# Optimization experiments

Measured on AMD Instinct MI355X. Metric: run time of the kernel, lower is better.

## Reference

```python
import jax, jax.numpy as jnp
from jax import lax
import numpy as np

T, B, IN, H = 512, 256, 128, 512
TAU_MIN, TAU_MAX, DT = 0.2, 2.0, 0.1


def setup_inputs() -> dict:
    key = jax.random.key(0)
    ks = jax.random.split(key, 7)
    s_zh = 1.0 / np.sqrt(IN + H)  # torch Linear default init scale (fan_in)
    s_h = 1.0 / np.sqrt(H)
    return {
        "x_seq": jax.random.normal(ks[0], (T, B, IN), dtype=jnp.float32),
        "Wc": jax.random.uniform(ks[1], (IN + H, H), jnp.float32, -s_zh, s_zh),
        "bc": jax.random.uniform(ks[2], (H,), jnp.float32, -s_zh, s_zh),
        "Wt": jax.random.uniform(ks[3], (IN + H, H), jnp.float32, -s_zh, s_zh),
        "bt": jax.random.uniform(ks[4], (H,), jnp.float32, -s_zh, s_zh),
        "Wo": jax.random.uniform(ks[5], (H, 1), jnp.float32, -s_h, s_h),
        "bo": jax.random.uniform(ks[6], (1,), jnp.float32, -s_h, s_h),
    }


def reference(x_seq, Wc, bc, Wt, bt, Wo, bo):
    # Liquid time-constant RNN: sequential scan over T timesteps.
    def step(h, x_t):
        z = jnp.concatenate([x_t, h], axis=-1)           # [B, IN+H]
        candidate = jnp.tanh(z @ Wc + bc)                # [B, H]
        tau = TAU_MIN + jax.nn.sigmoid(z @ Wt + bt) * (TAU_MAX - TAU_MIN)
        h_next = h + DT * (-h + candidate) / tau         # ODE Euler update
        y_t = h_next @ Wo + bo                           # [B, 1]
        return h_next, (y_t, tau)

    h0 = jnp.zeros((x_seq.shape[1], Wc.shape[1]), dtype=x_seq.dtype)
    _, (y_seq, tau_seq) = lax.scan(step, h0, x_seq)
    return y_seq, tau_seq
```

## Files before the change

### kernel.cpp

```cpp
#include <hip/hip_runtime.h>
#include <stdint.h>

#define T_STEPS 512
#define BATCH   256
#define INP     128
#define HID     512
#define BGN     16
#define CGN     8
#define RB      16
#define CB      64
#define ZP      648

typedef float f32x4 __attribute__((ext_vector_type(4)));
typedef short s16x8 __attribute__((ext_vector_type(8)));
typedef unsigned short u16;
typedef unsigned int   u32;
typedef unsigned long long u64;

__device__ __forceinline__ u32 f2bf(float f) {
  union { float f; u32 u; } v; v.f = f;
  return (v.u + 0x7fffu + ((v.u >> 16) & 1u)) >> 16;
}

__device__ __forceinline__ float bf2f(u16 b) {
  union { u32 u; float f; } v; v.u = ((u32)b) << 16;
  return v.f;
}


__global__ __launch_bounds__(256, 1)
void liquid_persistent(const float* __restrict__ x_seq,
                       const float* __restrict__ Wc, const float* __restrict__ bc,
                       const float* __restrict__ Wt, const float* __restrict__ bt,
                       const float* __restrict__ Wo, const float* __restrict__ bo,
                       float* __restrict__ y_out, float* __restrict__ tau_out,
                       u16* __restrict__ hb)
{
  const int tid  = threadIdx.x;
  const int l    = tid & 63;
  const int w    = tid >> 6;
  const int quad = l >> 4;
  const int ln   = l & 15;
  const int bg   = blockIdx.x & (BGN - 1);
  const int cg   = blockIdx.x >> 4;
  const int R0   = bg * RB;
  const int C0   = cg * CB;
  const int cn   = C0 + w * 16 + ln;

  __shared__ u16 zS[RB][ZP];
  __shared__ float ypS[4];

  s16x8 wfC[20], wfT[20];
#pragma unroll
  for (int kt = 0; kt < 20; ++kt) {
#pragma unroll
    for (int j = 0; j < 8; ++j) {
      int k = kt * 32 + quad * 8 + j;
      wfC[kt][j] = (short)f2bf(Wc[k * HID + cn]);
      wfT[kt][j] = (short)f2bf(Wt[k * HID + cn]);
    }
  }

  const float bcv = bc[cn], btv = bt[cn];
  const float bov = bo[0];
  float hm[4] = {0.f, 0.f, 0.f, 0.f};

  const int xrow = tid >> 4;
  const int xseg = tid & 15;

  const int yrow = 2 * cg + (w >> 1);
  const int yc0  = (w & 1) * 256 + l * 4;
  const float4 wo4 = *(const float4*)&Wo[yc0];

  int ii[7];
#pragma unroll
  for (int jx = 0; jx < 7; ++jx) ii[jx] = jx + (jx >= cg ? 1 : 0);

  const size_t rowq = HID / 4;
  u64* hbase = (u64*)(void*)hb;
  const size_t myrow = (size_t)(R0 + xrow) * rowq;

  {
    const float* xp = x_seq + ((size_t)0 * BATCH + R0 + xrow) * INP + xseg * 8;
    float4 a = *(const float4*)xp;
    float4 b = *(const float4*)(xp + 4);
    u64 w0 = (u64)f2bf(a.x) | ((u64)f2bf(a.y) << 16) |
             ((u64)f2bf(a.z) << 32) | ((u64)f2bf(a.w) << 48);
    u64 w1 = (u64)f2bf(b.x) | ((u64)f2bf(b.y) << 16) |
             ((u64)f2bf(b.z) << 32) | ((u64)f2bf(b.w) << 48);
    *(u64*)&zS[xrow][xseg * 8]     = w0;
    *(u64*)&zS[xrow][xseg * 8 + 4] = w1;
  }
  __syncthreads();

  for (int t = 0; t <= T_STEPS; ++t) {
    const u64* rbase = hbase + (size_t)(t & 3) * BATCH * rowq + myrow + xseg;

    u64 tmp[7];
    if (t > 0) {
#pragma unroll
      for (int jx = 0; jx < 7; ++jx)
        tmp[jx] = __hip_atomic_load(rbase + ii[jx] * 16, __ATOMIC_RELAXED,
                                    __HIP_MEMORY_SCOPE_AGENT);
    }

    f32x4 aC0 = {0.f,0.f,0.f,0.f}, aC1 = {0.f,0.f,0.f,0.f};
    f32x4 aT0 = {0.f,0.f,0.f,0.f}, aT1 = {0.f,0.f,0.f,0.f};
    const u16* zb = &zS[ln][quad * 8];
    if (t < T_STEPS) {
      s16x8 a0 = *(const s16x8*)(zb);
      s16x8 a1 = *(const s16x8*)(zb + 32);
      s16x8 a2 = *(const s16x8*)(zb + 64);
      s16x8 a3 = *(const s16x8*)(zb + 96);
      aC0 = __builtin_amdgcn_mfma_f32_16x16x32_bf16(a0, wfC[0], aC0, 0,0,0);
      aT0 = __builtin_amdgcn_mfma_f32_16x16x32_bf16(a0, wfT[0], aT0, 0,0,0);
      aC1 = __builtin_amdgcn_mfma_f32_16x16x32_bf16(a1, wfC[1], aC1, 0,0,0);
      aT1 = __builtin_amdgcn_mfma_f32_16x16x32_bf16(a1, wfT[1], aT1, 0,0,0);
      aC0 = __builtin_amdgcn_mfma_f32_16x16x32_bf16(a2, wfC[2], aC0, 0,0,0);
      aT0 = __builtin_amdgcn_mfma_f32_16x16x32_bf16(a2, wfT[2], aT0, 0,0,0);
      aC1 = __builtin_amdgcn_mfma_f32_16x16x32_bf16(a3, wfC[3], aC1, 0,0,0);
      aT1 = __builtin_amdgcn_mfma_f32_16x16x32_bf16(a3, wfT[3], aT1, 0,0,0);
    }

    u64 hv[7];
    if (t == 0) {
#pragma unroll
      for (int jx = 0; jx < 7; ++jx) hv[jx] = 0;
    } else {
      bool need[7];
      int pending = 0;
#pragma unroll
      for (int jx = 0; jx < 7; ++jx) {
        u64 v = tmp[jx];
        bool ok = ((u32)v != 0xFFFFFFFFu) && ((u32)(v >> 32) != 0xFFFFFFFFu);
        hv[jx] = v;
        need[jx] = !ok;
        pending += ok ? 0 : 1;
      }
      while (pending) {
#pragma unroll
        for (int jx = 0; jx < 7; ++jx)
          if (need[jx])
            tmp[jx] = __hip_atomic_load(rbase + ii[jx] * 16, __ATOMIC_RELAXED,
                                        __HIP_MEMORY_SCOPE_AGENT);
#pragma unroll
        for (int jx = 0; jx < 7; ++jx)
          if (need[jx]) {
            u64 v = tmp[jx];
            if (((u32)v != 0xFFFFFFFFu) && ((u32)(v >> 32) != 0xFFFFFFFFu)) {
              hv[jx] = v;
              need[jx] = false;
              --pending;
            }
          }
      }
    }

    if (t < T_STEPS) {
      u64* pp = hbase + (size_t)((t + 2) & 3) * BATCH * rowq + myrow
              + (C0 / 4 + xseg);
      __hip_atomic_store(pp, ~0ull, __ATOMIC_RELAXED, __HIP_MEMORY_SCOPE_AGENT);
    }

    float4 xr0, xr1;
    if (t < T_STEPS) {
      const int tn = (t + 1 < T_STEPS) ? t + 1 : t;
      const float* xp = x_seq + ((size_t)tn * BATCH + R0 + xrow) * INP + xseg * 8;
      xr0 = *(const float4*)xp;
      xr1 = *(const float4*)(xp + 4);
    }

#pragma unroll
    for (int jx = 0; jx < 7; ++jx)
      *(u64*)&zS[xrow][INP + (ii[jx] * 16 + xseg) * 4] = hv[jx];
#pragma unroll
    for (int r = 0; r < 4; ++r)
      zS[quad * 4 + r][INP + cn] = (u16)f2bf(hm[r]);

    __syncthreads();

    float tauv[4];
    if (t < T_STEPS) {
#pragma unroll
      for (int kt = 4; kt < 20; kt += 2) {
        s16x8 a0 = *(const s16x8*)(zb + kt * 32);
        s16x8 a1 = *(const s16x8*)(zb + kt * 32 + 32);
        aC0 = __builtin_amdgcn_mfma_f32_16x16x32_bf16(a0, wfC[kt],   aC0, 0,0,0);
        aT0 = __builtin_amdgcn_mfma_f32_16x16x32_bf16(a0, wfT[kt],   aT0, 0,0,0);
        aC1 = __builtin_amdgcn_mfma_f32_16x16x32_bf16(a1, wfC[kt+1], aC1, 0,0,0);
        aT1 = __builtin_amdgcn_mfma_f32_16x16x32_bf16(a1, wfT[kt+1], aT1, 0,0,0);
      }
      aC0 += aC1;
      aT0 += aT1;

      u64 w0 = (u64)f2bf(xr0.x) | ((u64)f2bf(xr0.y) << 16) |
               ((u64)f2bf(xr0.z) << 32) | ((u64)f2bf(xr0.w) << 48);
      u64 w1 = (u64)f2bf(xr1.x) | ((u64)f2bf(xr1.y) << 16) |
               ((u64)f2bf(xr1.z) << 32) | ((u64)f2bf(xr1.w) << 48);
      *(u64*)&zS[xrow][xseg * 8]     = w0;
      *(u64*)&zS[xrow][xseg * 8 + 4] = w1;

#pragma unroll
      for (int r = 0; r < 4; ++r) {
        float pc = aC0[r] + bcv;
        float pt = aT0[r] + btv;
        pc = fminf(fmaxf(pc, -20.f), 20.f);
        float e  = __expf(2.f * pc);
        float cand = (e - 1.f) / (e + 1.f);
        float tau  = 0.2f + 1.8f / (1.f + __expf(-pt));
        hm[r] += 0.1f * (cand - hm[r]) / tau;
        tauv[r] = tau;
      }

      asm volatile("s_waitcnt vmcnt(0)" ::: "memory");

#pragma unroll
      for (int r = 0; r < 4; ++r) {
        u32 bits = f2bf(hm[r]);
        u32 b0   = bits | ((u32)__shfl_xor((int)bits, 1) << 16);
        u64 q    = (u64)b0 | ((u64)(u32)__shfl_xor((int)b0, 2) << 32);
        if (!(ln & 3)) {
          u64* hp = hbase + (size_t)((t + 1) & 3) * BATCH * rowq
                  + (size_t)(R0 + quad * 4 + r) * rowq + (cn / 4);
          __hip_atomic_store(hp, q, __ATOMIC_RELAXED, __HIP_MEMORY_SCOPE_AGENT);
        }
      }
    }

    if (t > 0) {
      u64 hq = *(const u64*)&zS[yrow][INP + yc0];
      float py = bf2f((u16)hq)          * wo4.x
               + bf2f((u16)(hq >> 16))  * wo4.y
               + bf2f((u16)(hq >> 32))  * wo4.z
               + bf2f((u16)(hq >> 48))  * wo4.w;
      py += __shfl_down(py, 32);
      py += __shfl_down(py, 16);
      py += __shfl_down(py, 8);
      py += __shfl_down(py, 4);
      py += __shfl_down(py, 2);
      py += __shfl_down(py, 1);
      if (l == 0) ypS[w] = py;
    }

    __syncthreads();

    if (t > 0 && tid < 2) {
      float yv = ypS[tid * 2] + ypS[tid * 2 + 1] + bov;
      y_out[(size_t)(t - 1) * BATCH + R0 + 2 * cg + tid] = yv;
    }

    if (t < T_STEPS) {
#pragma unroll
      for (int r = 0; r < 4; ++r)
        __builtin_nontemporal_store(
            tauv[r],
            &tau_out[((size_t)t * BATCH + R0 + quad * 4 + r) * HID + cn]);
    }
  }
}

extern "C" void kernel_launch(void* const* d_in, const int* in_sizes, int n_in,
                              void* d_out, int out_size, void* d_ws, size_t ws_size,
                              hipStream_t stream) {
  (void)in_sizes; (void)n_in; (void)out_size; (void)ws_size;
  const float* x_seq = (const float*)d_in[0];
  const float* Wc    = (const float*)d_in[1];
  const float* bc    = (const float*)d_in[2];
  const float* Wt    = (const float*)d_in[3];
  const float* bt    = (const float*)d_in[4];
  const float* Wo    = (const float*)d_in[5];
  const float* bo    = (const float*)d_in[6];

  float* y_out   = (float*)d_out;
  float* tau_out = (float*)d_out + (size_t)T_STEPS * BATCH;

  const size_t HB_BYTES = (size_t)4 * BATCH * HID * sizeof(u16);
  u16* hb = (u16*)d_ws;

  hipMemsetAsync(d_ws, 0xFF, HB_BYTES, stream);

  liquid_persistent<<<dim3(BGN * CGN), dim3(256), 0, stream>>>(
      x_seq, Wc, bc, Wt, bt, Wo, bo, y_out, tau_out, hb);
}
```

Before: 1.961 ms.

## Add per-wave step flags for cross-block readiness and reorder step pipeline

Each wave publishes a step counter in a new flags array once its h stores have drained. Consumers now spin on these small counters instead of repeatedly re-polling the h data for the 0xFF sentinel, and reload only the still-missing words after a fence. The next-timestep x load is also hoisted ahead of the first MFMA batch, and its conversion into shared memory moves before the barrier. The y reduction is written one step later, which moves the block barrier and drops the trailing one. This adds flag traffic and an extra vmcnt wait per step, and relies on relaxed-ordering visibility of the flag relative to the data.

```diff
diff --git a/kernel.cpp b/kernel.cpp
--- a/kernel.cpp
+++ b/kernel.cpp
@@ -34,7 +34,7 @@
                        const float* __restrict__ Wt, const float* __restrict__ bt,
                        const float* __restrict__ Wo, const float* __restrict__ bo,
                        float* __restrict__ y_out, float* __restrict__ tau_out,
-                       u16* __restrict__ hb)
+                       u16* __restrict__ hb, int* __restrict__ flags)
 {
   const int tid  = threadIdx.x;
   const int l    = tid & 63;
@@ -67,6 +67,7 @@
 
   const int xrow = tid >> 4;
   const int xseg = tid & 15;
+  const int cw   = xseg >> 2;
 
   const int yrow = 2 * cg + (w >> 1);
   const int yc0  = (w & 1) * 256 + l * 4;
@@ -97,11 +98,23 @@
     const u64* rbase = hbase + (size_t)(t & 3) * BATCH * rowq + myrow + xseg;
 
     u64 tmp[7];
+    int cvt[7];
     if (t > 0) {
 #pragma unroll
       for (int jx = 0; jx < 7; ++jx)
         tmp[jx] = __hip_atomic_load(rbase + ii[jx] * 16, __ATOMIC_RELAXED,
                                     __HIP_MEMORY_SCOPE_AGENT);
+#pragma unroll
+      for (int jx = 0; jx < 7; ++jx)
+        cvt[jx] = __hip_atomic_load(&flags[(bg * CGN + ii[jx]) * 16 + cw * 4],
+                                    __ATOMIC_RELAXED, __HIP_MEMORY_SCOPE_AGENT);
+    }
+    float4 xr0, xr1;
+    if (t < T_STEPS) {
+      const int tn = (t + 1 < T_STEPS) ? t + 1 : t;
+      const float* xp = x_seq + ((size_t)tn * BATCH + R0 + xrow) * INP + xseg * 8;
+      xr0 = *(const float4*)xp;
+      xr1 = *(const float4*)(xp + 4);
     }
 
     f32x4 aC0 = {0.f,0.f,0.f,0.f}, aC1 = {0.f,0.f,0.f,0.f};
@@ -128,31 +141,45 @@
       for (int jx = 0; jx < 7; ++jx) hv[jx] = 0;
     } else {
       bool need[7];
-      int pending = 0;
 #pragma unroll
       for (int jx = 0; jx < 7; ++jx) {
         u64 v = tmp[jx];
         bool ok = ((u32)v != 0xFFFFFFFFu) && ((u32)(v >> 32) != 0xFFFFFFFFu);
         hv[jx] = v;
         need[jx] = !ok;
-        pending += ok ? 0 : 1;
-      }
-      while (pending) {
+      }
+      bool ready = true;
+#pragma unroll
+      for (int jx = 0; jx < 7; ++jx) ready = ready && (cvt[jx] >= t);
+      while (!ready) {
 #pragma unroll
         for (int jx = 0; jx < 7; ++jx)
-          if (need[jx])
-            tmp[jx] = __hip_atomic_load(rbase + ii[jx] * 16, __ATOMIC_RELAXED,
-                                        __HIP_MEMORY_SCOPE_AGENT);
+          cvt[jx] = __hip_atomic_load(&flags[(bg * CGN + ii[jx]) * 16 + cw * 4],
+                                      __ATOMIC_RELAXED, __HIP_MEMORY_SCOPE_AGENT);
 #pragma unroll
         for (int jx = 0; jx < 7; ++jx)
           if (need[jx]) {
-            u64 v = tmp[jx];
+            u64 v = __hip_atomic_load(rbase + ii[jx] * 16, __ATOMIC_RELAXED,
+                                      __HIP_MEMORY_SCOPE_AGENT);
             if (((u32)v != 0xFFFFFFFFu) && ((u32)(v >> 32) != 0xFFFFFFFFu)) {
               hv[jx] = v;
               need[jx] = false;
-              --pending;
             }
           }
+        ready = true;
+#pragma unroll
+        for (int jx = 0; jx < 7; ++jx) ready = ready && (cvt[jx] >= t);
+      }
+      int pend = 0;
+#pragma unroll
+      for (int jx = 0; jx < 7; ++jx) pend += need[jx] ? 1 : 0;
+      if (pend) {
+        __threadfence();
+#pragma unroll
+        for (int jx = 0; jx < 7; ++jx)
+          if (need[jx])
+            hv[jx] = __hip_atomic_load(rbase + ii[jx] * 16, __ATOMIC_RELAXED,
+                                       __HIP_MEMORY_SCOPE_AGENT);
       }
     }
 
@@ -162,13 +189,11 @@
       __hip_atomic_store(pp, ~0ull, __ATOMIC_RELAXED, __HIP_MEMORY_SCOPE_AGENT);
     }
 
-    float4 xr0, xr1;
-    if (t < T_STEPS) {
-      const int tn = (t + 1 < T_STEPS) ? t + 1 : t;
-      const float* xp = x_seq + ((size_t)tn * BATCH + R0 + xrow) * INP + xseg * 8;
-      xr0 = *(const float4*)xp;
-      xr1 = *(const float4*)(xp + 4);
-    }
+    __syncthreads();
+
+    if (t >= 2 && tid < 2)
+      y_out[(size_t)(t - 2) * BATCH + R0 + 2 * cg + tid] =
+          ypS[tid * 2] + ypS[tid * 2 + 1] + bov;
 
 #pragma unroll
     for (int jx = 0; jx < 7; ++jx)
@@ -176,10 +201,17 @@
 #pragma unroll
     for (int r = 0; r < 4; ++r)
       zS[quad * 4 + r][INP + cn] = (u16)f2bf(hm[r]);
+    if (t < T_STEPS) {
+      u64 w0 = (u64)f2bf(xr0.x) | ((u64)f2bf(xr0.y) << 16) |
+               ((u64)f2bf(xr0.z) << 32) | ((u64)f2bf(xr0.w) << 48);
+      u64 w1 = (u64)f2bf(xr1.x) | ((u64)f2bf(xr1.y) << 16) |
+               ((u64)f2bf(xr1.z) << 32) | ((u64)f2bf(xr1.w) << 48);
+      *(u64*)&zS[xrow][xseg * 8]     = w0;
+      *(u64*)&zS[xrow][xseg * 8 + 4] = w1;
+    }
 
     __syncthreads();
 
-    float tauv[4];
     if (t < T_STEPS) {
 #pragma unroll
       for (int kt = 4; kt < 20; kt += 2) {
@@ -193,13 +225,7 @@
       aC0 += aC1;
       aT0 += aT1;
 
-      u64 w0 = (u64)f2bf(xr0.x) | ((u64)f2bf(xr0.y) << 16) |
-               ((u64)f2bf(xr0.z) << 32) | ((u64)f2bf(xr0.w) << 48);
-      u64 w1 = (u64)f2bf(xr1.x) | ((u64)f2bf(xr1.y) << 16) |
-               ((u64)f2bf(xr1.z) << 32) | ((u64)f2bf(xr1.w) << 48);
-      *(u64*)&zS[xrow][xseg * 8]     = w0;
-      *(u64*)&zS[xrow][xseg * 8 + 4] = w1;
-
+      float tauv[4];
 #pragma unroll
       for (int r = 0; r < 4; ++r) {
         float pc = aC0[r] + bcv;
@@ -225,9 +251,20 @@
           __hip_atomic_store(hp, q, __ATOMIC_RELAXED, __HIP_MEMORY_SCOPE_AGENT);
         }
       }
-    }
-
-    if (t > 0) {
+
+      asm volatile("s_waitcnt vmcnt(0)" ::: "memory");
+      if (l == 0)
+        __hip_atomic_store(&flags[(bg * CGN + cg) * 16 + w * 4], t + 1,
+                           __ATOMIC_RELAXED, __HIP_MEMORY_SCOPE_AGENT);
+
+#pragma unroll
+      for (int r = 0; r < 4; ++r)
+        __builtin_nontemporal_store(
+            tauv[r],
+            &tau_out[((size_t)t * BATCH + R0 + quad * 4 + r) * HID + cn]);
+    }
+
+    {
       u64 hq = *(const u64*)&zS[yrow][INP + yc0];
       float py = bf2f((u16)hq)          * wo4.x
                + bf2f((u16)(hq >> 16))  * wo4.y
@@ -241,22 +278,12 @@
       py += __shfl_down(py, 1);
       if (l == 0) ypS[w] = py;
     }
-
-    __syncthreads();
-
-    if (t > 0 && tid < 2) {
-      float yv = ypS[tid * 2] + ypS[tid * 2 + 1] + bov;
-      y_out[(size_t)(t - 1) * BATCH + R0 + 2 * cg + tid] = yv;
-    }
-
-    if (t < T_STEPS) {
-#pragma unroll
-      for (int r = 0; r < 4; ++r)
-        __builtin_nontemporal_store(
-            tauv[r],
-            &tau_out[((size_t)t * BATCH + R0 + quad * 4 + r) * HID + cn]);
-    }
   }
+
+  __syncthreads();
+  if (tid < 2)
+    y_out[(size_t)(T_STEPS - 1) * BATCH + R0 + 2 * cg + tid] =
+        ypS[tid * 2] + ypS[tid * 2 + 1] + bov;
 }
 
 extern "C" void kernel_launch(void* const* d_in, const int* in_sizes, int n_in,
@@ -274,11 +301,13 @@
   float* y_out   = (float*)d_out;
   float* tau_out = (float*)d_out + (size_t)T_STEPS * BATCH;
 
-  const size_t HB_BYTES = (size_t)4 * BATCH * HID * sizeof(u16);
-  u16* hb = (u16*)d_ws;
-
-  hipMemsetAsync(d_ws, 0xFF, HB_BYTES, stream);
+  const size_t HB_BYTES   = (size_t)4 * BATCH * HID * sizeof(u16);
+  const size_t FLAG_BYTES = (size_t)BGN * CGN * 16 * sizeof(int);
+  u16* hb    = (u16*)d_ws;
+  int* flags = (int*)((char*)d_ws + HB_BYTES);
+
+  hipMemsetAsync(d_ws, 0xFF, HB_BYTES + FLAG_BYTES, stream);
 
   liquid_persistent<<<dim3(BGN * CGN), dim3(256), 0, stream>>>(
-      x_seq, Wc, bc, Wt, bt, Wo, bo, y_out, tau_out, hb);
+      x_seq, Wc, bc, Wt, bt, Wo, bo, y_out, tau_out, hb, flags);
 }
```

Result: no change. 1.953 ms (-0.4%).
